# Optimization experiments

Measured on AMD Instinct MI355X. Metric: run time of the kernel, lower is better.

Reference implementation:

```python
import jax, jax.numpy as jnp
import numpy as np

N_BUSES = 2000
W1, W2, W3, LMBDA = 1.0, 1.0, 1.0, 0.1


def setup_inputs() -> dict:
    key = jax.random.key(0)
    k0, k1, k2, k3, k4 = jax.random.split(key, 5)
    B, E = 32, 6000
    x = jax.random.normal(k0, (B * N_BUSES, 6), jnp.float32)
    edge_attr = jax.random.normal(k1, (B * E, 2), jnp.float32)
    edge_index = jax.random.randint(k2, (2, B * E), 0, N_BUSES)
    outputs = jax.random.normal(k3, (B * N_BUSES, 2), jnp.float32)
    labels = jax.random.normal(k4, (B * N_BUSES, 2), jnp.float32)
    return {"x": x, "edge_attr": edge_attr, "edge_index": edge_index,
            "outputs": outputs, "labels": labels}


def _physics_terms(x, edge_attr, edge_index, outputs):
    B = x.shape[0] // N_BUSES
    # Vpred: complex voltage prediction, (B, N, 1)
    Vpred = (outputs[:, 0] + 1j * outputs[:, 1]).astype(jnp.complex64)
    Vpred = Vpred.reshape(B, N_BUSES, 1)
    nf = x.reshape(B, N_BUSES, 6)
    ea = edge_attr.reshape(B, -1, 2)
    E = ea.shape[1]
    ei = edge_index.reshape(2, B, E) % N_BUSES  # (2, B, E)
    S = (nf[:, :, 0] + 1j * nf[:, :, 1]).astype(jnp.complex64)  # (B, N)
    Vm = nf[:, :, 2]
    bus_type = nf[:, :, 3:6]
    adm = (ea[:, :, 0] + 1j * ea[:, :, 1]).astype(jnp.complex64)  # (B, E)
    # scatter edge admittances into dense Y (B, N, N)
    b_idx = jnp.arange(B)[:, None]
    Y = jnp.zeros((B, N_BUSES, N_BUSES), jnp.complex64)
    Y = Y.at[b_idx, ei[0], ei[1]].set(adm)
    # Spred = V * conj(Y @ V)
    YV = jnp.matmul(Y, Vpred)                      # (B, N, 1)
    Spred = (Vpred * jnp.conj(YV))[:, :, 0]        # (B, N)
    S_mean = jnp.mean(S, axis=1, keepdims=True)
    S_inverse = jnp.where(S != 0, 1.0 / S, 1.0 / S_mean)
    S_inverse_norm = jnp.abs(S_inverse)
    result1 = ((Spred - S) ** 2) * bus_type[:, :, 0]                    # complex
    result2 = ((Spred.real - S.real) ** 2) * bus_type[:, :, 1]          # real
    Vm_mean = jnp.mean(Vm, axis=1, keepdims=True)
    Vm_inverse = jnp.where(Vm != 0, 1.0 / Vm, 1.0 / Vm_mean)
    D1 = S_inverse_norm * (result1 + result2)                           # complex
    Vmag = jnp.abs(Vpred[:, :, 0])
    D2 = jnp.abs(Vmag * (bus_type[:, :, 1] + bus_type[:, :, 2]) - Vm) * Vm_inverse
    D3 = jnp.abs(Vpred[:, :, 0].imag * bus_type[:, :, 2]) * Vm_inverse
    return jnp.mean(D1), jnp.mean(D2), jnp.mean(D3)


def reference(x, edge_attr, edge_index, outputs, labels):
    d1, d2, d3 = _physics_terms(x, edge_attr, edge_index, outputs)
    physics_loss = W1 * d1 + W2 * d2 + W3 * d3  # complex (D1 is complex, as in torch)
    mse = jnp.mean((outputs - labels) ** 2)
    loss = mse + LMBDA * physics_loss
    return loss, physics_loss, d1, d2, d3
```

## Files before the change

### kernel.cpp

```cpp
#include <hip/hip_runtime.h>

typedef unsigned long long ull;

#define N_BUSES     2000
#define BATCH       32
#define EDGES_PER_B 6000
#define TOTAL_BUSES (BATCH * N_BUSES)
#define TOTAL_EDGES (BATCH * EDGES_PER_B)

#define SPLIT   16
#define BUS_PER (N_BUSES / SPLIT)
#define TPB     1024
#define NBLOCKS (BATCH * SPLIT)
#define EPT     6

#define HBITS 10
#define HSIZE (1 << HBITS)
#define HMASK (HSIZE - 1)

__device__ __forceinline__ unsigned hash_key(int key) {
    return ((unsigned)key * 2654435761u) >> (32 - HBITS);
}

__global__ __launch_bounds__(TPB)
void fused_split(const float* __restrict__ x, const float* __restrict__ ea,
                 const int* __restrict__ ei, const float* __restrict__ outputs,
                 const float* __restrict__ labels, double* __restrict__ part) {
    __shared__ ull slots[HSIZE];
    __shared__ float yv_sh[2 * BUS_PER];
    __shared__ double red[5][TPB / 64];
    __shared__ double red2[3][TPB / 64];
    __shared__ float bst[3];
    __shared__ int pend[64];
    __shared__ int npend;

    const int blk = blockIdx.x;
    const int b = blk / SPLIT;
    const int p = blk % SPLIT;
    const int r0 = p * BUS_PER;
    const int tid = threadIdx.x;
    const int wave = tid >> 6, lane = tid & 63;

    int iv[EPT], jv[EPT];
#pragma unroll
    for (int k = 0; k < EPT; k++) {
        int e = tid + k * TPB;
        if (e < EDGES_PER_B) {
            iv[k] = ei[b * EDGES_PER_B + e];
            jv[k] = ei[TOTAL_EDGES + b * EDGES_PER_B + e];
        } else { iv[k] = -1; jv[k] = 0; }
    }

    slots[tid] = 0ULL;
    if (tid < 2 * BUS_PER) yv_sh[tid] = 0.0f;
    if (tid == 0) npend = 0;
    __syncthreads();

#pragma unroll
    for (int k = 0; k < EPT; k++) {
        int e = tid + k * TPB;
        if (iv[k] < 0) continue;
        int i = iv[k] % N_BUSES;
        if (i < r0 || i >= r0 + BUS_PER) continue;
        int j = jv[k] % N_BUSES;
        int key = i * N_BUSES + j;
        ull tag = (ull)(unsigned)(key + 1) << 13;
        ull packed = tag | (unsigned)e;
        unsigned h = hash_key(key);
        int deposed = -1;
        bool we_add = false;
        while (true) {
            ull old = atomicCAS(&slots[h], 0ULL, packed);
            if (old == 0ULL) { we_add = true; break; }
            if ((old >> 13) == (ull)(unsigned)(key + 1)) {
                ull prev = atomicMax(&slots[h], packed);
                if (prev < packed) { we_add = true; deposed = (int)(prev & 0x1FFFULL); }
                break;
            }
            h = (h + 1) & HMASK;
        }
        if (we_add) {
            float2 v = ((const float2*)outputs)[b * N_BUSES + j];
            float2 a = ((const float2*)ea)[b * EDGES_PER_B + e];
            float addr = a.x * v.x - a.y * v.y;
            float addi = a.x * v.y + a.y * v.x;
            if (deposed >= 0) {
                float2 ap = ((const float2*)ea)[b * EDGES_PER_B + deposed];
                addr -= ap.x * v.x - ap.y * v.y;
                addi -= ap.x * v.y + ap.y * v.x;
            }
            int il = i - r0;
            atomicAdd(&yv_sh[2 * il],     addr);
            atomicAdd(&yv_sh[2 * il + 1], addi);
        }
    }
    __syncthreads();

    double t0 = 0.0, t1 = 0.0, t2 = 0.0, t3 = 0.0, t4 = 0.0;
    if (tid < BUS_PER) {
        int il = tid;
        int idx = b * N_BUSES + r0 + il;
        const float2* row2 = (const float2*)(x + (size_t)idx * 6);
        float2 q0 = row2[0], q1 = row2[1], q2 = row2[2];
        float sre = q0.x, sim = q0.y, Vm = q1.x;
        float bt0 = q1.y, bt1 = q2.x, bt2 = q2.y;
        if ((sre == 0.0f && sim == 0.0f) || Vm == 0.0f) {
            int pp = atomicAdd(&npend, 1);
            if (pp < 64) pend[pp] = il;
        } else {
            float2 v = ((const float2*)outputs)[idx];
            float yvr = yv_sh[2 * il], yvi = yv_sh[2 * il + 1];
            float spr = v.x * yvr + v.y * yvi;
            float spi = v.y * yvr - v.x * yvi;
            float den = sre * sre + sim * sim;
            float ir = sre / den, ii = -sim / den;
            float sinv_norm = sqrtf(ir * ir + ii * ii);
            float cr = spr - sre, ci = spi - sim;
            t0 = (double)(sinv_norm * ((cr * cr - ci * ci) * bt0 + (cr * cr) * bt1));
            t1 = (double)(sinv_norm * (2.0f * cr * ci * bt0));
            float vminv = 1.0f / Vm;
            float vmag = sqrtf(v.x * v.x + v.y * v.y);
            t2 = (double)(fabsf(vmag * (bt1 + bt2) - Vm) * vminv);
            t3 = (double)(fabsf(v.y * bt2) * vminv);
            float2 l = ((const float2*)labels)[idx];
            float e0 = v.x - l.x, e1 = v.y - l.y;
            t4 = (double)(e0 * e0 + e1 * e1);
        }
    }
    for (int off = 32; off > 0; off >>= 1) {
        t0 += __shfl_down(t0, off, 64);
        t1 += __shfl_down(t1, off, 64);
        t2 += __shfl_down(t2, off, 64);
        t3 += __shfl_down(t3, off, 64);
        t4 += __shfl_down(t4, off, 64);
    }
    if (lane == 0) {
        red[0][wave] = t0; red[1][wave] = t1; red[2][wave] = t2;
        red[3][wave] = t3; red[4][wave] = t4;
    }
    __syncthreads();

    double a0 = 0, a1 = 0, a2 = 0, a3 = 0, a4 = 0;
    if (tid == 0) {
        for (int w = 0; w < TPB / 64; w++) {
            a0 += red[0][w]; a1 += red[1][w]; a2 += red[2][w];
            a3 += red[3][w]; a4 += red[4][w];
        }
    }

    if (npend > 0) {
        double sre = 0.0, sim = 0.0, svm = 0.0;
        for (int i = tid; i < N_BUSES; i += TPB) {
            const float* row = x + (size_t)(b * N_BUSES + i) * 6;
            sre += (double)row[0];
            sim += (double)row[1];
            svm += (double)row[2];
        }
        for (int off = 32; off > 0; off >>= 1) {
            sre += __shfl_down(sre, off, 64);
            sim += __shfl_down(sim, off, 64);
            svm += __shfl_down(svm, off, 64);
        }
        if (lane == 0) { red2[0][wave] = sre; red2[1][wave] = sim; red2[2][wave] = svm; }
        __syncthreads();
        if (tid == 0) {
            double sa = 0, sb = 0, sc = 0;
            for (int w = 0; w < TPB / 64; w++) { sa += red2[0][w]; sb += red2[1][w]; sc += red2[2][w]; }
            bst[0] = (float)(sa / N_BUSES);
            bst[1] = (float)(sb / N_BUSES);
            bst[2] = (float)(sc / N_BUSES);
        }
        __syncthreads();
        if (tid == 0) {
            int np = npend < 64 ? npend : 64;
            for (int q = 0; q < np; q++) {
                int il = pend[q];
                int idx = b * N_BUSES + r0 + il;
                const float2* row2 = (const float2*)(x + (size_t)idx * 6);
                float2 q0 = row2[0], q1 = row2[1], q2 = row2[2];
                float sr = q0.x, si = q0.y, Vm = q1.x;
                float bt0 = q1.y, bt1 = q2.x, bt2 = q2.y;
                float2 v = ((const float2*)outputs)[idx];
                float yvr = yv_sh[2 * il], yvi = yv_sh[2 * il + 1];
                float spr = v.x * yvr + v.y * yvi;
                float spi = v.y * yvr - v.x * yvi;
                float ir, ii;
                if (sr != 0.0f || si != 0.0f) {
                    float den = sr * sr + si * si;
                    ir = sr / den; ii = -si / den;
                } else {
                    float mr = bst[0], mi = bst[1];
                    float den = mr * mr + mi * mi;
                    ir = mr / den; ii = -mi / den;
                }
                float sinv_norm = sqrtf(ir * ir + ii * ii);
                float cr = spr - sr, ci = spi - si;
                a0 += (double)(sinv_norm * ((cr * cr - ci * ci) * bt0 + (cr * cr) * bt1));
                a1 += (double)(sinv_norm * (2.0f * cr * ci * bt0));
                float vminv = (Vm != 0.0f) ? (1.0f / Vm) : (1.0f / bst[2]);
                float vmag = sqrtf(v.x * v.x + v.y * v.y);
                a2 += (double)(fabsf(vmag * (bt1 + bt2) - Vm) * vminv);
                a3 += (double)(fabsf(v.y * bt2) * vminv);
                float2 l = ((const float2*)labels)[idx];
                float e0 = v.x - l.x, e1 = v.y - l.y;
                a4 += (double)(e0 * e0 + e1 * e1);
            }
        }
    }

    if (tid == 0) {
        part[blk * 5 + 0] = a0; part[blk * 5 + 1] = a1; part[blk * 5 + 2] = a2;
        part[blk * 5 + 3] = a3; part[blk * 5 + 4] = a4;
    }
}

__global__ __launch_bounds__(512)
void finalize(const double* __restrict__ part, float* __restrict__ out, int out_size) {
    int tid = threadIdx.x;
    int wave = tid >> 6, lane = tid & 63;
    double v0 = part[tid * 5 + 0], v1 = part[tid * 5 + 1], v2 = part[tid * 5 + 2];
    double v3 = part[tid * 5 + 3], v4 = part[tid * 5 + 4];
    for (int off = 32; off > 0; off >>= 1) {
        v0 += __shfl_down(v0, off, 64);
        v1 += __shfl_down(v1, off, 64);
        v2 += __shfl_down(v2, off, 64);
        v3 += __shfl_down(v3, off, 64);
        v4 += __shfl_down(v4, off, 64);
    }
    __shared__ double sh[5][8];
    if (lane == 0) {
        sh[0][wave] = v0; sh[1][wave] = v1; sh[2][wave] = v2;
        sh[3][wave] = v3; sh[4][wave] = v4;
    }
    __syncthreads();
    if (tid == 0) {
        double a0 = 0, a1 = 0, a2 = 0, a3 = 0, a4 = 0;
        for (int w = 0; w < 8; w++) {
            a0 += sh[0][w]; a1 += sh[1][w]; a2 += sh[2][w];
            a3 += sh[3][w]; a4 += sh[4][w];
        }
        double inv = 1.0 / (double)TOTAL_BUSES;
        double d1re = a0 * inv, d1im = a1 * inv;
        double d2 = a2 * inv, d3 = a3 * inv;
        double mse = a4 / (2.0 * (double)TOTAL_BUSES);
        double phre = d1re + d2 + d3, phim = d1im;
        double lre = mse + 0.1 * phre, lim = 0.1 * phim;
        if (out_size == 8) {
            out[0] = (float)lre;  out[1] = (float)lim;
            out[2] = (float)phre; out[3] = (float)phim;
            out[4] = (float)d1re; out[5] = (float)d1im;
            out[6] = (float)d2;   out[7] = (float)d3;
        } else {
            float vals[5] = {(float)lre, (float)phre, (float)d1re, (float)d2, (float)d3};
            int n = out_size < 5 ? out_size : 5;
            for (int k = 0; k < n; k++) out[k] = vals[k];
            for (int k = 5; k < out_size && k < 64; k++) out[k] = 0.0f;
        }
    }
}

extern "C" void kernel_launch(void* const* d_in, const int* in_sizes, int n_in,
                              void* d_out, int out_size, void* d_ws, size_t ws_size,
                              hipStream_t stream) {
    const float* x       = (const float*)d_in[0];
    const float* ea      = (const float*)d_in[1];
    const int*   ei      = (const int*)d_in[2];
    const float* outputs = (const float*)d_in[3];
    const float* labels  = (const float*)d_in[4];
    double* part = (double*)d_ws;

    fused_split<<<NBLOCKS, TPB, 0, stream>>>(x, ea, ei, outputs, labels, part);
    finalize<<<1, 512, 0, stream>>>(part, (float*)d_out, out_size);
}
```

Baseline: 84.30 us.

## Halve block split per batch and prefetch edge/bus data before hashing

Reduces the per-batch split from 16 to 8 blocks, so each block handles 250 buses, and doubles the shared hash table to 2048 slots. This cuts redundant reads of the full edge index per batch, since each block previously scanned all 6000 edges to keep only 1/16 of them. Per-bus x, outputs and labels, plus admittance and voltage values for in-range edges, are now loaded up front before the hash phase so their latency overlaps the table init and barrier. The trade-off is fewer blocks (256 instead of 512), which lowers parallelism on a large GPU, and more register pressure from the prefetched arrays.

New measurement: 83.61 us. No clear change (-0.8%).

```diff
diff --git a/kernel.cpp b/kernel.cpp
--- a/kernel.cpp
+++ b/kernel.cpp
@@ -8,13 +8,13 @@
 #define TOTAL_BUSES (BATCH * N_BUSES)
 #define TOTAL_EDGES (BATCH * EDGES_PER_B)
 
-#define SPLIT   16
+#define SPLIT   8
 #define BUS_PER (N_BUSES / SPLIT)
 #define TPB     1024
 #define NBLOCKS (BATCH * SPLIT)
 #define EPT     6
 
-#define HBITS 10
+#define HBITS 11
 #define HSIZE (1 << HBITS)
 #define HMASK (HSIZE - 1)
 
@@ -41,28 +41,47 @@
     const int tid = threadIdx.x;
     const int wave = tid >> 6, lane = tid & 63;
 
+    float2 q0, q1, q2, vP, lP;
+    const int idxP = b * N_BUSES + r0 + tid;
+    if (tid < BUS_PER) {
+        const float2* row2 = (const float2*)(x + (size_t)idxP * 6);
+        q0 = row2[0]; q1 = row2[1]; q2 = row2[2];
+        vP = ((const float2*)outputs)[idxP];
+        lP = ((const float2*)labels)[idxP];
+    }
+
     int iv[EPT], jv[EPT];
 #pragma unroll
     for (int k = 0; k < EPT; k++) {
         int e = tid + k * TPB;
         if (e < EDGES_PER_B) {
-            iv[k] = ei[b * EDGES_PER_B + e];
-            jv[k] = ei[TOTAL_EDGES + b * EDGES_PER_B + e];
+            iv[k] = ei[b * EDGES_PER_B + e] % N_BUSES;
+            jv[k] = ei[TOTAL_EDGES + b * EDGES_PER_B + e] % N_BUSES;
         } else { iv[k] = -1; jv[k] = 0; }
     }
+    float2 av[EPT], vv[EPT];
+    bool inr[EPT];
+#pragma unroll
+    for (int k = 0; k < EPT; k++) {
+        int i = iv[k];
+        inr[k] = (i >= r0) && (i < r0 + BUS_PER);
+        if (inr[k]) {
+            av[k] = ((const float2*)ea)[b * EDGES_PER_B + tid + k * TPB];
+            vv[k] = ((const float2*)outputs)[b * N_BUSES + jv[k]];
+        }
+    }
 
     slots[tid] = 0ULL;
+    slots[tid + TPB] = 0ULL;
     if (tid < 2 * BUS_PER) yv_sh[tid] = 0.0f;
     if (tid == 0) npend = 0;
     __syncthreads();
 
 #pragma unroll
     for (int k = 0; k < EPT; k++) {
+        if (!inr[k]) continue;
         int e = tid + k * TPB;
-        if (iv[k] < 0) continue;
-        int i = iv[k] % N_BUSES;
-        if (i < r0 || i >= r0 + BUS_PER) continue;
-        int j = jv[k] % N_BUSES;
+        int i = iv[k], j = jv[k];
         int key = i * N_BUSES + j;
         ull tag = (ull)(unsigned)(key + 1) << 13;
         ull packed = tag | (unsigned)e;
@@ -80,8 +99,7 @@
             h = (h + 1) & HMASK;
         }
         if (we_add) {
-            float2 v = ((const float2*)outputs)[b * N_BUSES + j];
-            float2 a = ((const float2*)ea)[b * EDGES_PER_B + e];
+            float2 a = av[k], v = vv[k];
             float addr = a.x * v.x - a.y * v.y;
             float addi = a.x * v.y + a.y * v.x;
             if (deposed >= 0) {
@@ -99,19 +117,15 @@
     double t0 = 0.0, t1 = 0.0, t2 = 0.0, t3 = 0.0, t4 = 0.0;
     if (tid < BUS_PER) {
         int il = tid;
-        int idx = b * N_BUSES + r0 + il;
-        const float2* row2 = (const float2*)(x + (size_t)idx * 6);
-        float2 q0 = row2[0], q1 = row2[1], q2 = row2[2];
         float sre = q0.x, sim = q0.y, Vm = q1.x;
         float bt0 = q1.y, bt1 = q2.x, bt2 = q2.y;
         if ((sre == 0.0f && sim == 0.0f) || Vm == 0.0f) {
             int pp = atomicAdd(&npend, 1);
             if (pp < 64) pend[pp] = il;
         } else {
-            float2 v = ((const float2*)outputs)[idx];
             float yvr = yv_sh[2 * il], yvi = yv_sh[2 * il + 1];
-            float spr = v.x * yvr + v.y * yvi;
-            float spi = v.y * yvr - v.x * yvi;
+            float spr = vP.x * yvr + vP.y * yvi;
+            float spi = vP.y * yvr - vP.x * yvi;
             float den = sre * sre + sim * sim;
             float ir = sre / den, ii = -sim / den;
             float sinv_norm = sqrtf(ir * ir + ii * ii);
@@ -119,11 +133,10 @@
             t0 = (double)(sinv_norm * ((cr * cr - ci * ci) * bt0 + (cr * cr) * bt1));
             t1 = (double)(sinv_norm * (2.0f * cr * ci * bt0));
             float vminv = 1.0f / Vm;
-            float vmag = sqrtf(v.x * v.x + v.y * v.y);
+            float vmag = sqrtf(vP.x * vP.x + vP.y * vP.y);
             t2 = (double)(fabsf(vmag * (bt1 + bt2) - Vm) * vminv);
-            t3 = (double)(fabsf(v.y * bt2) * vminv);
-            float2 l = ((const float2*)labels)[idx];
-            float e0 = v.x - l.x, e1 = v.y - l.y;
+            t3 = (double)(fabsf(vP.y * bt2) * vminv);
+            float e0 = vP.x - lP.x, e1 = vP.y - lP.y;
             t4 = (double)(e0 * e0 + e1 * e1);
         }
     }
@@ -177,9 +190,9 @@
                 int il = pend[q];
                 int idx = b * N_BUSES + r0 + il;
                 const float2* row2 = (const float2*)(x + (size_t)idx * 6);
-                float2 q0 = row2[0], q1 = row2[1], q2 = row2[2];
-                float sr = q0.x, si = q0.y, Vm = q1.x;
-                float bt0 = q1.y, bt1 = q2.x, bt2 = q2.y;
+                float2 w0 = row2[0], w1 = row2[1], w2 = row2[2];
+                float sr = w0.x, si = w0.y, Vm = w1.x;
+                float bt0 = w1.y, bt1 = w2.x, bt2 = w2.y;
                 float2 v = ((const float2*)outputs)[idx];
                 float yvr = yv_sh[2 * il], yvi = yv_sh[2 * il + 1];
                 float spr = v.x * yvr + v.y * yvi;
@@ -214,7 +227,7 @@
     }
 }
 
-__global__ __launch_bounds__(512)
+__global__ __launch_bounds__(256)
 void finalize(const double* __restrict__ part, float* __restrict__ out, int out_size) {
     int tid = threadIdx.x;
     int wave = tid >> 6, lane = tid & 63;
@@ -227,7 +240,7 @@
         v3 += __shfl_down(v3, off, 64);
         v4 += __shfl_down(v4, off, 64);
     }
-    __shared__ double sh[5][8];
+    __shared__ double sh[5][4];
     if (lane == 0) {
         sh[0][wave] = v0; sh[1][wave] = v1; sh[2][wave] = v2;
         sh[3][wave] = v3; sh[4][wave] = v4;
@@ -235,7 +248,7 @@
     __syncthreads();
     if (tid == 0) {
         double a0 = 0, a1 = 0, a2 = 0, a3 = 0, a4 = 0;
-        for (int w = 0; w < 8; w++) {
+        for (int w = 0; w < 4; w++) {
             a0 += sh[0][w]; a1 += sh[1][w]; a2 += sh[2][w];
             a3 += sh[3][w]; a4 += sh[4][w];
         }
@@ -270,5 +283,5 @@
     double* part = (double*)d_ws;
 
     fused_split<<<NBLOCKS, TPB, 0, stream>>>(x, ea, ei, outputs, labels, part);
-    finalize<<<1, 512, 0, stream>>>(part, (float*)d_out, out_size);
-}
+    finalize<<<1, 256, 0, stream>>>(part, (float*)d_out, out_size);
+}
```
